# Optimization experiments

Hardware: AMD Instinct MI355X
Metric: run time of the kernel (lower is better)

Reference implementation:

```python
import jax, jax.numpy as jnp
import numpy as np

D_MODEL = 512
D_STATE = 64
BATCH = 8
SEQ_L = 4096


def setup_inputs() -> dict:
    key = jax.random.key(0)
    k_u, k_c, k_d = jax.random.split(key, 3)
    u = jax.random.normal(k_u, (BATCH, D_MODEL, SEQ_L), dtype=jnp.float32)
    # B buffer: zeros with first state column = 1 (fixed shift-SSM input matrix)
    B = jnp.zeros((D_MODEL, D_STATE), dtype=jnp.float32).at[:, 0].set(1.0)
    C = jax.random.normal(k_c, (1, D_MODEL, D_STATE), dtype=jnp.float32)
    D = jax.random.normal(k_d, (D_MODEL,), dtype=jnp.float32)
    return {"u": u, "B": B, "C": C, "D": D}


def reference(u, B, C, D):
    """Shift state-space layer. u: (batch, H, L) -> (batch, H, L)."""
    L = u.shape[-1]
    n = 2 * L  # pad to 2L so circular conv == linear (causal) conv
    B_fc = jnp.conj(jnp.fft.rfft(B, n=n))            # (H, n//2+1)
    C_f = jnp.fft.rfft(C, n=n)                       # (1, H, n//2+1)
    kernel = jnp.fft.irfft(B_fc * C_f, n=n)[..., :L]  # (1, H, L)
    kernel_f = jnp.fft.rfft(kernel, n=n)             # (1, H, n//2+1)
    u_f = jnp.fft.rfft(u, n=n)                       # (batch, H, n//2+1)
    y = jnp.fft.irfft(u_f * kernel_f, n=n)[..., :L]  # (batch, H, L)
    return y + u * D[:, None]
```

## Files before the change

kernel.cpp:

```cpp
#include <hip/hip_runtime.h>
#include <hip/hip_bf16.h>


#define D_MODEL 512
#define D_STATE 64
#define BATCH   8
#define SEQ_L   4096
#define NT      256

typedef short           s16x8 __attribute__((ext_vector_type(8)));
typedef unsigned short  u16;
typedef unsigned int    u32;
typedef u32             u32x2 __attribute__((ext_vector_type(2)));
typedef u32             u32x4 __attribute__((ext_vector_type(4)));
typedef float           f32x4 __attribute__((ext_vector_type(4)));

__device__ __forceinline__ int SW(int g) { return g ^ ((g >> 3) & 7); }

__device__ __forceinline__ u32 cvt_pk(float lo, float hi) {
    u32 r;
    asm("v_cvt_pk_bf16_f32 %0, %1, %2" : "=v"(r) : "v"(lo), "v"(hi));
    return r;
}

__global__ void __launch_bounds__(NT)
shift_mfma(const float* __restrict__ u, const float* __restrict__ B,
           const float* __restrict__ C, const float* __restrict__ D,
           float* __restrict__ y) {
    const int row = blockIdx.x;
    const int h   = row & (D_MODEL - 1);
    const float* __restrict__ urow = u + (size_t)row * SEQ_L;
    float* __restrict__ yrow       = y + (size_t)row * SEQ_L;

    __shared__ u16   ub[536 * 8];
    __shared__ float Bs[64];
    __shared__ float Cs[128];
    __shared__ float Kf[64];

    const int t = threadIdx.x;

    if (t < 16) {
        ((float4*)Bs)[t] = ((const float4*)(B + h * D_STATE))[t];
    } else if (t < 48) {
        const int j = t - 16;
        ((float4*)Cs)[j] = (j < 16) ? ((const float4*)(C + h * D_STATE))[j]
                                    : make_float4(0.f, 0.f, 0.f, 0.f);
    }

    const float4 v0 = *(const float4*)(urow + 4 * t + 0);
    const float4 v1 = *(const float4*)(urow + 4 * t + 1024);
    const float4 v2 = *(const float4*)(urow + 4 * t + 2048);
    const float4 v3 = *(const float4*)(urow + 4 * t + 3072);
    {
        const float4 vv[4] = {v0, v1, v2, v3};
        #pragma unroll
        for (int j = 0; j < 4; ++j) {
            u32x2 pk = { cvt_pk(vv[j].x, vv[j].y), cvt_pk(vv[j].z, vv[j].w) };
            const int byte = 128 + 8 * t + 2048 * j;
            const int sb   = (SW(byte >> 4) << 4) | (byte & 8);
            *(u32x2*)((char*)ub + sb) = pk;
        }
    }
    if (t < 8) {
        u32x4 z = {0, 0, 0, 0};
        *(u32x4*)((char*)ub + (SW(t) << 4)) = z;
    } else if (t < 20) {
        u32x4 z = {0, 0, 0, 0};
        const int g = 520 + (t - 8);
        *(u32x4*)((char*)ub + (SW(g) << 4)) = z;
    }
    __syncthreads();

    if (t < D_STATE) {
        float s0 = 0.f, s1 = 0.f, s2 = 0.f, s3 = 0.f;
        #pragma unroll
        for (int j = 0; j < D_STATE; j += 4) {
            s0 = fmaf(Bs[j + 0], Cs[t + j + 0], s0);
            s1 = fmaf(Bs[j + 1], Cs[t + j + 1], s1);
            s2 = fmaf(Bs[j + 2], Cs[t + j + 2], s2);
            s3 = fmaf(Bs[j + 3], Cs[t + j + 3], s3);
        }
        float s = (s0 + s1) + (s2 + s3);
        if (t == 0) s += D[h];
        Kf[t] = s;
    }
    __syncthreads();

    const int l  = t & 63;
    const int n  = l & 15;
    const int q  = l >> 4;
    const int pm = ((n & 3) << 2) | (n >> 2);
    u32x4 bfr[3];
    #pragma unroll
    for (int c = 0; c < 3; ++c) {
        float tv[8];
        #pragma unroll
        for (int j = 0; j < 8; ++j) {
            const int p = 32 * c + 8 * q + j;
            const int k = 64 + n - p;
            tv[j] = (k >= 0 && k < D_STATE) ? Kf[k] : 0.f;
        }
        #pragma unroll
        for (int w = 0; w < 4; ++w) bfr[c][w] = cvt_pk(tv[2 * w], tv[2 * w + 1]);
    }

    const int wbase = 1024 * (t >> 6);
    #pragma unroll
    for (int tt = 0; tt < 4; ++tt) {
        const int base = wbase + 256 * tt;
        f32x4 acc = {0.f, 0.f, 0.f, 0.f};
        #pragma unroll
        for (int c = 0; c < 3; ++c) {
            const int L  = base + 16 * pm + 32 * c + 8 * q;
            const int sb = SW(L >> 3) << 4;
            const s16x8 a = *(const s16x8*)((const char*)ub + sb);
            acc = __builtin_amdgcn_mfma_f32_16x16x32_bf16(
                      a, __builtin_bit_cast(s16x8, bfr[c]), acc, 0, 0, 0);
        }
        #pragma unroll
        for (int r = 0; r < 4; ++r)
            yrow[base + 64 * r + 16 * q + n] = acc[r];
    }
}

extern "C" void kernel_launch(void* const* d_in, const int* in_sizes, int n_in,
                              void* d_out, int out_size, void* d_ws, size_t ws_size,
                              hipStream_t stream) {
    const float* u = (const float*)d_in[0];
    const float* B = (const float*)d_in[1];
    const float* C = (const float*)d_in[2];
    const float* D = (const float*)d_in[3];
    float* y = (float*)d_out;

    shift_mfma<<<dim3(BATCH * D_MODEL), dim3(NT), 0, stream>>>(u, B, C, D, y);
}
```

Baseline: 120.0 us.

## Process two rows per block and swap MFMA operands for vectorized stores

Each block now handles two (batch, channel) rows that share the same channel, so the kernel setup (B/C loads, Kf computation, Toeplitz fragment build) is amortized over twice the work and the grid is halved. All eight row loads are issued up front, before the parameter loads, to increase memory-level parallelism. The MFMA operands are swapped so the Toeplitz fragment is the A operand, which lets each lane write its accumulator as one contiguous float4 store instead of four strided scalar stores. The cost is double the LDS per block and more live registers, which may reduce occupancy.

```diff
diff --git a/kernel.cpp b/kernel.cpp
--- a/kernel.cpp
+++ b/kernel.cpp
@@ -1,5 +1,4 @@
 #include <hip/hip_runtime.h>
-#include <hip/hip_bf16.h>
 
 
 #define D_MODEL 512
@@ -7,6 +6,8 @@
 #define BATCH   8
 #define SEQ_L   4096
 #define NT      256
+#define NBLK    2048
+#define CH      536
 
 typedef short           s16x8 __attribute__((ext_vector_type(8)));
 typedef unsigned short  u16;
@@ -27,17 +28,28 @@
 shift_mfma(const float* __restrict__ u, const float* __restrict__ B,
            const float* __restrict__ C, const float* __restrict__ D,
            float* __restrict__ y) {
-    const int row = blockIdx.x;
-    const int h   = row & (D_MODEL - 1);
-    const float* __restrict__ urow = u + (size_t)row * SEQ_L;
-    float* __restrict__ yrow       = y + (size_t)row * SEQ_L;
+    const int bid = blockIdx.x;
+    const int h   = bid & (D_MODEL - 1);
+    const float* __restrict__ ur0 = u + (size_t)bid * SEQ_L;
+    const float* __restrict__ ur1 = u + (size_t)(bid + NBLK) * SEQ_L;
+    float* __restrict__ yr0       = y + (size_t)bid * SEQ_L;
+    float* __restrict__ yr1       = y + (size_t)(bid + NBLK) * SEQ_L;
 
-    __shared__ u16   ub[536 * 8];
+    __shared__ u16   ub[2 * CH * 8];
     __shared__ float Bs[64];
     __shared__ float Cs[128];
     __shared__ float Kf[64];
 
     const int t = threadIdx.x;
+
+    const float4 v0 = *(const float4*)(ur0 + 4 * t + 0);
+    const float4 v1 = *(const float4*)(ur0 + 4 * t + 1024);
+    const float4 v2 = *(const float4*)(ur0 + 4 * t + 2048);
+    const float4 v3 = *(const float4*)(ur0 + 4 * t + 3072);
+    const float4 w0 = *(const float4*)(ur1 + 4 * t + 0);
+    const float4 w1 = *(const float4*)(ur1 + 4 * t + 1024);
+    const float4 w2 = *(const float4*)(ur1 + 4 * t + 2048);
+    const float4 w3 = *(const float4*)(ur1 + 4 * t + 3072);
 
     if (t < 16) {
         ((float4*)Bs)[t] = ((const float4*)(B + h * D_STATE))[t];
@@ -47,27 +59,26 @@
                                     : make_float4(0.f, 0.f, 0.f, 0.f);
     }
 
-    const float4 v0 = *(const float4*)(urow + 4 * t + 0);
-    const float4 v1 = *(const float4*)(urow + 4 * t + 1024);
-    const float4 v2 = *(const float4*)(urow + 4 * t + 2048);
-    const float4 v3 = *(const float4*)(urow + 4 * t + 3072);
     {
-        const float4 vv[4] = {v0, v1, v2, v3};
+        const float4 vv[8] = {v0, v1, v2, v3, w0, w1, w2, w3};
         #pragma unroll
-        for (int j = 0; j < 4; ++j) {
+        for (int j = 0; j < 8; ++j) {
             u32x2 pk = { cvt_pk(vv[j].x, vv[j].y), cvt_pk(vv[j].z, vv[j].w) };
-            const int byte = 128 + 8 * t + 2048 * j;
+            const int byte = 128 + 8 * t + 2048 * (j & 3);
             const int sb   = (SW(byte >> 4) << 4) | (byte & 8);
-            *(u32x2*)((char*)ub + sb) = pk;
+            *(u32x2*)((char*)ub + (j >> 2) * (CH * 16) + sb) = pk;
         }
     }
-    if (t < 8) {
-        u32x4 z = {0, 0, 0, 0};
-        *(u32x4*)((char*)ub + (SW(t) << 4)) = z;
-    } else if (t < 20) {
-        u32x4 z = {0, 0, 0, 0};
-        const int g = 520 + (t - 8);
-        *(u32x4*)((char*)ub + (SW(g) << 4)) = z;
+    {
+        const u32x4 z = {0, 0, 0, 0};
+        if (t < 8)
+            *(u32x4*)((char*)ub + (SW(t) << 4)) = z;
+        else if (t < 16)
+            *(u32x4*)((char*)ub + CH * 16 + (SW(t - 8) << 4)) = z;
+        else if (t < 28)
+            *(u32x4*)((char*)ub + (SW(520 + t - 16) << 4)) = z;
+        else if (t < 40)
+            *(u32x4*)((char*)ub + CH * 16 + (SW(520 + t - 28) << 4)) = z;
     }
     __syncthreads();
 
@@ -86,40 +97,41 @@
     }
     __syncthreads();
 
-    const int l  = t & 63;
-    const int n  = l & 15;
-    const int q  = l >> 4;
-    const int pm = ((n & 3) << 2) | (n >> 2);
-    u32x4 bfr[3];
+    const int l = t & 63;
+    const int n = l & 15;
+    const int q = l >> 4;
+    u32x4 afr[3];
     #pragma unroll
     for (int c = 0; c < 3; ++c) {
         float tv[8];
         #pragma unroll
         for (int j = 0; j < 8; ++j) {
-            const int p = 32 * c + 8 * q + j;
-            const int k = 64 + n - p;
+            const int k = n + 64 - (32 * c + 8 * q + j);
             tv[j] = (k >= 0 && k < D_STATE) ? Kf[k] : 0.f;
         }
         #pragma unroll
-        for (int w = 0; w < 4; ++w) bfr[c][w] = cvt_pk(tv[2 * w], tv[2 * w + 1]);
+        for (int w = 0; w < 4; ++w) afr[c][w] = cvt_pk(tv[2 * w], tv[2 * w + 1]);
     }
 
     const int wbase = 1024 * (t >> 6);
     #pragma unroll
-    for (int tt = 0; tt < 4; ++tt) {
-        const int base = wbase + 256 * tt;
-        f32x4 acc = {0.f, 0.f, 0.f, 0.f};
+    for (int rr = 0; rr < 2; ++rr) {
+        const char* ubase = (const char*)ub + rr * (CH * 16);
+        float* __restrict__ yr = rr ? yr1 : yr0;
         #pragma unroll
-        for (int c = 0; c < 3; ++c) {
-            const int L  = base + 16 * pm + 32 * c + 8 * q;
-            const int sb = SW(L >> 3) << 4;
-            const s16x8 a = *(const s16x8*)((const char*)ub + sb);
-            acc = __builtin_amdgcn_mfma_f32_16x16x32_bf16(
-                      a, __builtin_bit_cast(s16x8, bfr[c]), acc, 0, 0, 0);
+        for (int tt = 0; tt < 4; ++tt) {
+            const int base = wbase + 256 * tt;
+            f32x4 acc = {0.f, 0.f, 0.f, 0.f};
+            #pragma unroll
+            for (int c = 0; c < 3; ++c) {
+                const int E  = base + 16 * n + 8 * q + 32 * c;
+                const int sb = SW(E >> 3) << 4;
+                const s16x8 b = *(const s16x8*)(ubase + sb);
+                acc = __builtin_amdgcn_mfma_f32_16x16x32_bf16(
+                          __builtin_bit_cast(s16x8, afr[c]), b, acc, 0, 0, 0);
+            }
+            *(f32x4*)(yr + base + 16 * n + 4 * q) = acc;
         }
-        #pragma unroll
-        for (int r = 0; r < 4; ++r)
-            yrow[base + 64 * r + 16 * q + n] = acc[r];
     }
 }
 
@@ -132,5 +144,5 @@
     const float* D = (const float*)d_in[3];
     float* y = (float*)d_out;
 
-    shift_mfma<<<dim3(BATCH * D_MODEL), dim3(NT), 0, stream>>>(u, B, C, D, y);
+    shift_mfma<<<dim3(NBLK), dim3(NT), 0, stream>>>(u, B, C, D, y);
 }
```

New measurement: 119.9 us. About the same (-0.1%).
